# Performance work log

Hardware: AMD Instinct MI355X
Metric: run time of the kernel (lower is better)

## Reference

```python
import jax, jax.numpy as jnp
import numpy as np

PI = np.pi
NDIMS, K, M, F = 3, 513, 65536, 16
H = (K - 1) // 2  # 256; augmented factor has K = 2*H + 1 rows


def setup_inputs() -> dict:
    key = jax.random.key(0)
    k1, k2, k3, k4 = jax.random.split(key, 4)
    x = jax.random.uniform(k1, (M, NDIMS), dtype=jnp.float32)          # samples in [0,1]
    factors_real = jax.random.uniform(k2, (NDIMS, H, F), dtype=jnp.float32)
    factors_imag = 0.1 * jax.random.uniform(k3, (NDIMS, H, F), dtype=jnp.float32)
    lam = jnp.full((F,), 1.0 / F, dtype=jnp.float32)                   # f_vec init in torch
    return {"x": x, "factors_real": factors_real, "factors_imag": factors_imag, "lam": lam}


def _augment(fr, fi):
    # aug_fac real = [R; ones; flip(R)], imag = [I; zeros; -flip(I)]  -> (NDIMS, K, F)
    ones = jnp.ones((NDIMS, 1, F), fr.dtype)
    zeros = jnp.zeros((NDIMS, 1, F), fi.dtype)
    Ar = jnp.concatenate([fr, ones, jnp.flip(fr, axis=1)], axis=1)
    Ai = jnp.concatenate([fi, zeros, -jnp.flip(fi, axis=1)], axis=1)
    return Ar, Ai


def _conditionals(Ar, Ai):
    # c[n, f] = 1 / trapz(relu(Re(bb1^T aug_fac_n))[:, f], t),  t = linspace(0.01, 1, 100)
    T = 100
    t = jnp.linspace(0.01, 1.0, T, dtype=jnp.float32)
    kv = jnp.arange(-H, H + 1, dtype=jnp.float32)
    phi = (2.0 * PI) * kv[:, None] * t[None, :]                         # (K, T)
    # bb1 = exp(-i*phi): Re(bb1^T (Ar + i Ai)) = cos(phi)^T Ar + sin(phi)^T Ai
    y = (jnp.einsum('kt,nkf->ntf', jnp.cos(phi), Ar)
         + jnp.einsum('kt,nkf->ntf', jnp.sin(phi), Ai))
    y = jnp.maximum(y, 0.0)
    dt = jnp.float32((1.0 - 0.01) / (T - 1))
    integral = 0.5 * jnp.sum(y[:, 1:, :] + y[:, :-1, :], axis=1) * dt   # (NDIMS, F)
    return 1.0 / integral


def reference(x, factors_real, factors_imag, lam):
    Ar, Ai = _augment(factors_real, factors_imag)
    # torch computes c from detached data (numpy trapz) -> constant w.r.t. grads
    c = jax.lax.stop_gradient(_conditionals(Ar, Ai))                    # (NDIMS, F)
    kv = jnp.arange(-H, H + 1, dtype=jnp.float32)
    # basis = exp(-i*2pi*k*x): Re(basis^T A) = cos^T Ar + sin^T Ai
    theta = (2.0 * PI) * kv[None, :, None] * jnp.swapaxes(x, 0, 1)[:, None, :]  # (NDIMS, K, M)
    proj = (jnp.einsum('nkm,nkf->nmf', jnp.cos(theta), Ar)
            + jnp.einsum('nkm,nkf->nmf', jnp.sin(theta), Ai))           # (NDIMS, M, F)
    proj = jnp.maximum(proj, 0.0) * c[:, None, :]
    res = jnp.prod(proj, axis=0)                                        # (M, F)
    # sum(res @ diagflat(lam), dim=1) == res @ lam
    return res @ lam
```

## Files before the change

### kernel.cpp

```cpp
#include <hip/hip_runtime.h>

#define NDIMS 3
#define H_HALF 256
#define F_DIM 16
#define PI_F 3.14159265358979323846f

typedef _Float16 half8_t __attribute__((ext_vector_type(8)));
typedef _Float16 h2 __attribute__((ext_vector_type(2)));
typedef __fp16 pk2_t __attribute__((ext_vector_type(2)));
typedef float float4_t __attribute__((ext_vector_type(4)));

#if __has_builtin(__builtin_amdgcn_fractf)
#define FRACT1(u) __builtin_amdgcn_fractf(u)
#else
#define FRACT1(u) ((u) - floorf(u))
#endif
#if __has_builtin(__builtin_amdgcn_sinf)
#define SIN2PI(u) __builtin_amdgcn_sinf(u)
#define COS2PI(u) __builtin_amdgcn_cosf(u)
#else
#define SIN2PI(u) __sinf(6.283185307f * (u))
#define COS2PI(u) __cosf(6.283185307f * (u))
#endif

static __device__ __forceinline__ unsigned int pk(float lo, float hi) {
    const pk2_t p = __builtin_amdgcn_cvt_pkrtz(lo, hi);
    return __builtin_bit_cast(unsigned int, p);
}
static __device__ __forceinline__ h2 pkh(float lo, float hi) {
    const pk2_t p = __builtin_amdgcn_cvt_pkrtz(lo, hi);
    return __builtin_bit_cast(h2, p);
}

static __device__ __forceinline__ float4_t tile_pass(const float xq,
                                                     const unsigned int* __restrict__ Brow,
                                                     const int q) {
    const float u1 = FRACT1(xq);
    const float cd1 = COS2PI(u1), sd1 = SIN2PI(u1);
    const float cd2 = fmaf(cd1, cd1, -sd1 * sd1), sd2 = 2.f * sd1 * cd1;
    const float cd3 = fmaf(cd2, cd1, -sd2 * sd1), sd3 = fmaf(sd2, cd1, cd2 * sd1);
    const h2 cc1 = pkh(cd1, cd1), ns1 = pkh(-sd1, sd1);
    const h2 cc2 = pkh(cd2, cd2), ns2 = pkh(-sd2, sd2);
    const h2 cc3 = pkh(cd3, cd3), ns3 = pkh(-sd3, sd3);
    const float ud = FRACT1(16.f * xq);
    const float cD = COS2PI(ud), sD = SIN2PI(ud);
    const float v0 = FRACT1((float)(q * 4 + 1) * xq);
    float c0 = COS2PI(v0), s0 = SIN2PI(v0);

    float4_t acc = {0.f, 0.f, 0.f, 0.f};
    #pragma unroll
    for (int s = 0; s < 16; ++s) {
        const int4 bv = *reinterpret_cast<const int4*>(Brow + s * 16);
        const half8_t bfrag = __builtin_bit_cast(half8_t, bv);
        const h2 b0 = pkh(c0, s0);
        const h2 bsw = pkh(s0, c0);
        const h2 d1 = __builtin_elementwise_fma(bsw, ns1, b0 * cc1);
        const h2 d2 = __builtin_elementwise_fma(bsw, ns2, b0 * cc2);
        const h2 d3 = __builtin_elementwise_fma(bsw, ns3, b0 * cc3);
        const int4 av = { __builtin_bit_cast(int, b0), __builtin_bit_cast(int, d1),
                          __builtin_bit_cast(int, d2), __builtin_bit_cast(int, d3) };
        const half8_t afrag = __builtin_bit_cast(half8_t, av);
        acc = __builtin_amdgcn_mfma_f32_16x16x32_f16(afrag, bfrag, acc, 0, 0, 0);
        const float t0 = fmaf(c0, cD, -s0 * sD);
        s0 = fmaf(s0, cD, c0 * sD);
        c0 = t0;
    }
    return acc;
}

__global__ __launch_bounds__(512, 4) void main_kernel(const float* __restrict__ x,
                                                      const float* __restrict__ fr,
                                                      const float* __restrict__ fi,
                                                      const float* __restrict__ lam,
                                                      float* __restrict__ out) {
    __shared__ __align__(16) unsigned int Bls[48 * 260];
    __shared__ float red[NDIMS][7][16];
    const int tid = threadIdx.x;

    {
        const float4* fr4 = (const float4*)fr;
        const float4* fi4 = (const float4*)fi;
        #pragma unroll
        for (int r = 0; r < 6; ++r) {
            const int i4 = r * 512 + tid;
            const float4 a = fr4[i4];
            const float4 b = fi4[i4];
            const int n = i4 >> 10;
            const int h = (i4 >> 2) & 255;
            const int f0 = (i4 & 3) * 4;
            const int base = (n * 16 + f0) * 260 + (255 - h);
            Bls[base      ] = pk(a.x, -b.x);
            Bls[base + 260] = pk(a.y, -b.y);
            Bls[base + 520] = pk(a.z, -b.z);
            Bls[base + 780] = pk(a.w, -b.w);
        }
    }
    __syncthreads();

    const int wave = tid >> 6;
    const int lane = tid & 63;
    const int l15 = lane & 15;
    const int q = lane >> 4;
    const int mbase = (blockIdx.x * 8 + wave) * 16;

    const float xv0 = x[(mbase + l15) * 3 + 0];
    const float xv1 = x[(mbase + l15) * 3 + 1];
    const float xv2 = x[(mbase + l15) * 3 + 2];
    const float lamv = lam[l15];

    if (wave < 7) {
        const float tv = 0.01f + 0.01f * (float)(wave * 16 + l15);
        #pragma unroll
        for (int n = 0; n < 3; ++n) {
            const unsigned int* Brow = &Bls[(n * 16 + l15) * 260 + q * 4];
            const float4_t ca = tile_pass(tv, Brow, q);
            float contrib = 0.f;
            #pragma unroll
            for (int i = 0; i < 4; ++i) {
                const int ti = wave * 16 + q * 4 + i;
                const float y = fmaxf(fmaf(2.f, ca[i], 1.f), 0.f);
                const float w = (ti == 0 || ti == 99) ? 0.005f
                                                      : (ti < 100 ? 0.01f : 0.f);
                contrib = fmaf(w, y, contrib);
            }
            contrib += __shfl_xor(contrib, 16, 64);
            contrib += __shfl_xor(contrib, 32, 64);
            if (lane < 16) red[n][wave][lane] = contrib;
        }
    }

    float4_t accs[3];
    #pragma unroll
    for (int n = 0; n < 3; ++n) {
        const float xq = (n == 0) ? xv0 : (n == 1 ? xv1 : xv2);
        const unsigned int* Brow = &Bls[(n * 16 + l15) * 260 + q * 4];
        accs[n] = tile_pass(xq, Brow, q);
    }

    __syncthreads();

    float cinv[3];
    #pragma unroll
    for (int n = 0; n < 3; ++n) {
        float s = 0.f;
        #pragma unroll
        for (int w = 0; w < 7; ++w) s += red[n][w][l15];
        cinv[n] = 1.f / s;
    }

    float r0 = 1.f, r1 = 1.f, r2 = 1.f, r3 = 1.f;
    #pragma unroll
    for (int n = 0; n < 3; ++n) {
        const float cc = cinv[n];
        r0 *= fmaxf(fmaf(2.f, accs[n][0], 1.f), 0.f) * cc;
        r1 *= fmaxf(fmaf(2.f, accs[n][1], 1.f), 0.f) * cc;
        r2 *= fmaxf(fmaf(2.f, accs[n][2], 1.f), 0.f) * cc;
        r3 *= fmaxf(fmaf(2.f, accs[n][3], 1.f), 0.f) * cc;
    }
    r0 *= lamv; r1 *= lamv; r2 *= lamv; r3 *= lamv;
    #pragma unroll
    for (int off = 1; off < 16; off <<= 1) {
        r0 += __shfl_xor(r0, off, 64);
        r1 += __shfl_xor(r1, off, 64);
        r2 += __shfl_xor(r2, off, 64);
        r3 += __shfl_xor(r3, off, 64);
    }
    if (l15 == 0) {
        float4 o = { r0, r1, r2, r3 };
        *reinterpret_cast<float4*>(out + mbase + q * 4) = o;
    }
}

extern "C" void kernel_launch(void* const* d_in, const int* in_sizes, int n_in,
                              void* d_out, int out_size, void* d_ws, size_t ws_size,
                              hipStream_t stream) {
    const float* x   = (const float*)d_in[0];
    const float* fr  = (const float*)d_in[1];
    const float* fi  = (const float*)d_in[2];
    const float* lam = (const float*)d_in[3];
    float* out = (float*)d_out;
    (void)d_ws; (void)ws_size;

    const int M = in_sizes[0] / NDIMS;

    main_kernel<<<M / 128, 512, 0, stream>>>(x, fr, fi, lam, out);
}
```

Measured before the change: 71.10 us.

## Interleave all three dimension chains and conditional pass in one MFMA loop

Replaces six sequential tile passes (three conditional, three projection) with a single 16-step loop that advances all three dimension recurrences, plus the t-grid recurrence, together. Each B fragment is loaded from LDS once per step and shared between the projection MFMA and the conditional MFMA. The conditional pass now reuses the t-grid A fragment across all three dimensions instead of rebuilding it three times. This exposes independent MFMA chains to hide MFMA latency and cuts redundant sincos and LDS work. In exchange it raises live register pressure (six accumulators, four chains) under 512-thread launch bounds, which risks spills or lower occupancy.

```diff
diff --git a/kernel.cpp b/kernel.cpp
--- a/kernel.cpp
+++ b/kernel.cpp
@@ -32,40 +32,40 @@
     return __builtin_bit_cast(h2, p);
 }
 
-static __device__ __forceinline__ float4_t tile_pass(const float xq,
-                                                     const unsigned int* __restrict__ Brow,
-                                                     const int q) {
-    const float u1 = FRACT1(xq);
+struct Chain {
+    float c0, s0;
+    float cD, sD;
+    h2 cc1, ns1, cc2, ns2, cc3, ns3;
+};
+
+static __device__ __forceinline__ Chain make_chain(const float v, const int q) {
+    Chain ch;
+    const float u1 = FRACT1(v);
     const float cd1 = COS2PI(u1), sd1 = SIN2PI(u1);
     const float cd2 = fmaf(cd1, cd1, -sd1 * sd1), sd2 = 2.f * sd1 * cd1;
     const float cd3 = fmaf(cd2, cd1, -sd2 * sd1), sd3 = fmaf(sd2, cd1, cd2 * sd1);
-    const h2 cc1 = pkh(cd1, cd1), ns1 = pkh(-sd1, sd1);
-    const h2 cc2 = pkh(cd2, cd2), ns2 = pkh(-sd2, sd2);
-    const h2 cc3 = pkh(cd3, cd3), ns3 = pkh(-sd3, sd3);
-    const float ud = FRACT1(16.f * xq);
-    const float cD = COS2PI(ud), sD = SIN2PI(ud);
-    const float v0 = FRACT1((float)(q * 4 + 1) * xq);
-    float c0 = COS2PI(v0), s0 = SIN2PI(v0);
-
-    float4_t acc = {0.f, 0.f, 0.f, 0.f};
-    #pragma unroll
-    for (int s = 0; s < 16; ++s) {
-        const int4 bv = *reinterpret_cast<const int4*>(Brow + s * 16);
-        const half8_t bfrag = __builtin_bit_cast(half8_t, bv);
-        const h2 b0 = pkh(c0, s0);
-        const h2 bsw = pkh(s0, c0);
-        const h2 d1 = __builtin_elementwise_fma(bsw, ns1, b0 * cc1);
-        const h2 d2 = __builtin_elementwise_fma(bsw, ns2, b0 * cc2);
-        const h2 d3 = __builtin_elementwise_fma(bsw, ns3, b0 * cc3);
-        const int4 av = { __builtin_bit_cast(int, b0), __builtin_bit_cast(int, d1),
-                          __builtin_bit_cast(int, d2), __builtin_bit_cast(int, d3) };
-        const half8_t afrag = __builtin_bit_cast(half8_t, av);
-        acc = __builtin_amdgcn_mfma_f32_16x16x32_f16(afrag, bfrag, acc, 0, 0, 0);
-        const float t0 = fmaf(c0, cD, -s0 * sD);
-        s0 = fmaf(s0, cD, c0 * sD);
-        c0 = t0;
-    }
-    return acc;
+    ch.cc1 = pkh(cd1, cd1); ch.ns1 = pkh(-sd1, sd1);
+    ch.cc2 = pkh(cd2, cd2); ch.ns2 = pkh(-sd2, sd2);
+    ch.cc3 = pkh(cd3, cd3); ch.ns3 = pkh(-sd3, sd3);
+    const float ud = FRACT1(16.f * v);
+    ch.cD = COS2PI(ud); ch.sD = SIN2PI(ud);
+    const float v0 = FRACT1((float)(q * 4 + 1) * v);
+    ch.c0 = COS2PI(v0); ch.s0 = SIN2PI(v0);
+    return ch;
+}
+
+static __device__ __forceinline__ half8_t step_afrag(Chain& ch) {
+    const h2 b0 = pkh(ch.c0, ch.s0);
+    const h2 bsw = pkh(ch.s0, ch.c0);
+    const h2 d1 = __builtin_elementwise_fma(bsw, ch.ns1, b0 * ch.cc1);
+    const h2 d2 = __builtin_elementwise_fma(bsw, ch.ns2, b0 * ch.cc2);
+    const h2 d3 = __builtin_elementwise_fma(bsw, ch.ns3, b0 * ch.cc3);
+    const int4 av = { __builtin_bit_cast(int, b0), __builtin_bit_cast(int, d1),
+                      __builtin_bit_cast(int, d2), __builtin_bit_cast(int, d3) };
+    const float t0 = fmaf(ch.c0, ch.cD, -ch.s0 * ch.sD);
+    ch.s0 = fmaf(ch.s0, ch.cD, ch.c0 * ch.sD);
+    ch.c0 = t0;
+    return __builtin_bit_cast(half8_t, av);
 }
 
 __global__ __launch_bounds__(512, 4) void main_kernel(const float* __restrict__ x,
@@ -102,18 +102,53 @@
     const int l15 = lane & 15;
     const int q = lane >> 4;
     const int mbase = (blockIdx.x * 8 + wave) * 16;
+    const bool condw = (wave < 7);
 
     const float xv0 = x[(mbase + l15) * 3 + 0];
     const float xv1 = x[(mbase + l15) * 3 + 1];
     const float xv2 = x[(mbase + l15) * 3 + 2];
     const float lamv = lam[l15];
 
-    if (wave < 7) {
-        const float tv = 0.01f + 0.01f * (float)(wave * 16 + l15);
+    Chain ch0 = make_chain(xv0, q);
+    Chain ch1 = make_chain(xv1, q);
+    Chain ch2 = make_chain(xv2, q);
+    Chain chT;
+    const float tv = 0.01f + 0.01f * (float)(wave * 16 + l15);
+    if (condw) chT = make_chain(tv, q);
+
+    const unsigned int* B0 = &Bls[(0 * 16 + l15) * 260 + q * 4];
+    const unsigned int* B1 = B0 + 16 * 260;
+    const unsigned int* B2 = B0 + 32 * 260;
+
+    float4_t aP0 = {0.f, 0.f, 0.f, 0.f}, aP1 = aP0, aP2 = aP0;
+    float4_t aC0 = aP0, aC1 = aP0, aC2 = aP0;
+
+    #pragma unroll
+    for (int s = 0; s < 16; ++s) {
+        const int4 bv0 = *reinterpret_cast<const int4*>(B0 + s * 16);
+        const int4 bv1 = *reinterpret_cast<const int4*>(B1 + s * 16);
+        const int4 bv2 = *reinterpret_cast<const int4*>(B2 + s * 16);
+        const half8_t bf0 = __builtin_bit_cast(half8_t, bv0);
+        const half8_t bf1 = __builtin_bit_cast(half8_t, bv1);
+        const half8_t bf2 = __builtin_bit_cast(half8_t, bv2);
+        const half8_t af0 = step_afrag(ch0);
+        aP0 = __builtin_amdgcn_mfma_f32_16x16x32_f16(af0, bf0, aP0, 0, 0, 0);
+        const half8_t af1 = step_afrag(ch1);
+        aP1 = __builtin_amdgcn_mfma_f32_16x16x32_f16(af1, bf1, aP1, 0, 0, 0);
+        const half8_t af2 = step_afrag(ch2);
+        aP2 = __builtin_amdgcn_mfma_f32_16x16x32_f16(af2, bf2, aP2, 0, 0, 0);
+        if (condw) {
+            const half8_t afT = step_afrag(chT);
+            aC0 = __builtin_amdgcn_mfma_f32_16x16x32_f16(afT, bf0, aC0, 0, 0, 0);
+            aC1 = __builtin_amdgcn_mfma_f32_16x16x32_f16(afT, bf1, aC1, 0, 0, 0);
+            aC2 = __builtin_amdgcn_mfma_f32_16x16x32_f16(afT, bf2, aC2, 0, 0, 0);
+        }
+    }
+
+    if (condw) {
         #pragma unroll
         for (int n = 0; n < 3; ++n) {
-            const unsigned int* Brow = &Bls[(n * 16 + l15) * 260 + q * 4];
-            const float4_t ca = tile_pass(tv, Brow, q);
+            const float4_t ca = (n == 0) ? aC0 : (n == 1 ? aC1 : aC2);
             float contrib = 0.f;
             #pragma unroll
             for (int i = 0; i < 4; ++i) {
@@ -129,14 +164,6 @@
         }
     }
 
-    float4_t accs[3];
-    #pragma unroll
-    for (int n = 0; n < 3; ++n) {
-        const float xq = (n == 0) ? xv0 : (n == 1 ? xv1 : xv2);
-        const unsigned int* Brow = &Bls[(n * 16 + l15) * 260 + q * 4];
-        accs[n] = tile_pass(xq, Brow, q);
-    }
-
     __syncthreads();
 
     float cinv[3];
@@ -151,11 +178,12 @@
     float r0 = 1.f, r1 = 1.f, r2 = 1.f, r3 = 1.f;
     #pragma unroll
     for (int n = 0; n < 3; ++n) {
+        const float4_t ap = (n == 0) ? aP0 : (n == 1 ? aP1 : aP2);
         const float cc = cinv[n];
-        r0 *= fmaxf(fmaf(2.f, accs[n][0], 1.f), 0.f) * cc;
-        r1 *= fmaxf(fmaf(2.f, accs[n][1], 1.f), 0.f) * cc;
-        r2 *= fmaxf(fmaf(2.f, accs[n][2], 1.f), 0.f) * cc;
-        r3 *= fmaxf(fmaf(2.f, accs[n][3], 1.f), 0.f) * cc;
+        r0 *= fmaxf(fmaf(2.f, ap[0], 1.f), 0.f) * cc;
+        r1 *= fmaxf(fmaf(2.f, ap[1], 1.f), 0.f) * cc;
+        r2 *= fmaxf(fmaf(2.f, ap[2], 1.f), 0.f) * cc;
+        r3 *= fmaxf(fmaf(2.f, ap[3], 1.f), 0.f) * cc;
     }
     r0 *= lamv; r1 *= lamv; r2 *= lamv; r3 *= lamv;
     #pragma unroll
```

After: 69.79 us. No clear change (-1.8%).
